# Kernel tuning notes

Measured on AMD Instinct MI355X. Metric: run time of the kernel, lower is better.

Reference implementation:

```python
import jax, jax.numpy as jnp
import numpy as np

B, D, H, W = 1024, 256, 8, 8
NS, ITERS, HID = 8, 5, 256  # HID = max(dim, 128)
EPS = 1e-8


def _ln(x, w, b, axes):
    mu = x.mean(axes, keepdims=True)
    var = x.var(axes, keepdims=True)
    return (x - mu) * jax.lax.rsqrt(var + 1e-5) * w + b


def _grid():
    ranges = [np.linspace(0.0, 1.0, num=r) for r in (H, W)]
    g = np.stack(np.meshgrid(*ranges, indexing='ij'), -1).reshape(H, W, -1)[None].astype(np.float32)
    return jnp.asarray(np.concatenate([g, 1.0 - g], -1))  # [1,H,W,4]


def setup_inputs():
    key = jax.random.key(0)
    ks = jax.random.split(key, 16)
    r = lambda i, shape, s=0.02: jax.random.normal(ks[i], shape, jnp.float32) * s
    d = D
    return {
        'inputs': jax.random.normal(ks[0], (B, D, H, W), jnp.float32),
        'slots_noise': jax.random.normal(ks[1], (B, NS, D), jnp.float32),
        'pos_W': r(2, (4, d)), 'pos_b': jnp.zeros((d,), jnp.float32),
        'enln_w': jnp.ones((H * W, d), jnp.float32), 'enln_b': jnp.zeros((H * W, d), jnp.float32),
        'f1W': r(3, (d, d)), 'f1b': jnp.zeros((d,), jnp.float32),
        'f2W': r(4, (d, d)), 'f2b': jnp.zeros((d,), jnp.float32),
        'ni_w': jnp.ones((d,), jnp.float32), 'ni_b': jnp.zeros((d,), jnp.float32),
        'qW': r(5, (d, d)), 'qb': jnp.zeros((d,), jnp.float32),
        'kW': r(6, (d, d)), 'kb': jnp.zeros((d,), jnp.float32),
        'vW': r(7, (d, d)), 'vb': jnp.zeros((d,), jnp.float32),
        'gih': r(8, (3 * d, d)), 'ghh': r(9, (3 * d, d)),
        'bih': jnp.zeros((3 * d,), jnp.float32), 'bhh': jnp.zeros((3 * d,), jnp.float32),
        'ns_w': jnp.ones((d,), jnp.float32), 'ns_b': jnp.zeros((d,), jnp.float32),
        'pf_w': jnp.ones((d,), jnp.float32), 'pf_b': jnp.zeros((d,), jnp.float32),
        'm1W': r(10, (d, HID)), 'm1b': jnp.zeros((HID,), jnp.float32),
        'm2W': r(11, (HID, d)), 'm2b': jnp.zeros((d,), jnp.float32),
        'slots_mu': r(12, (1, 1, d), 0.1),
        'slots_sigma': r(13, (1, 1, d), 0.1),
    }


def reference(inputs, slots_noise, pos_W, pos_b, enln_w, enln_b, f1W, f1b, f2W, f2b,
              ni_w, ni_b, qW, qb, kW, kb, vW, vb, gih, ghh, bih, bhh,
              ns_w, ns_b, pf_w, pf_b, m1W, m1b, m2W, m2b, slots_mu, slots_sigma):
    b, d = inputs.shape[0], inputs.shape[1]
    scale = d ** -0.5
    # encoder_transformation (position=True)
    x = jnp.transpose(inputs, (0, 2, 3, 1))          # [B,H,W,D]
    x = x + (_grid() @ pos_W + pos_b)                # SoftPositionEmbed
    x = x.reshape(b, H * W, d)                       # flatten spatial -> tokens
    x = _ln(x, enln_w, enln_b, (-2, -1))             # LayerNorm([ntokens, dim])
    x = jax.nn.relu(x @ f1W + f1b)
    x = jax.nn.relu(x @ f2W + f2b)
    x = _ln(x, ni_w, ni_b, (-1,))                    # norm_input
    k = x @ kW + kb                                  # [B,N,D]
    v = x @ vW + vb
    # slot init: torch.normal(mu, exp(0.5*sigma)) with explicit noise
    slots = slots_mu + jnp.exp(0.5 * slots_sigma) * slots_noise  # [B,S,D]
    for _ in range(ITERS):
        slots_prev = slots
        q = _ln(slots, ns_w, ns_b, (-1,)) @ qW + qb
        dots = jnp.einsum('bid,bjd->bij', q, k) * scale  # [B,S,N]
        attn = jax.nn.softmax(dots, axis=1) + EPS        # softmax over SLOT axis
        attn = attn / attn.sum(-1, keepdims=True)        # renormalize over tokens
        updates = jnp.einsum('bjd,bij->bid', v, attn)    # [B,S,D]
        # GRUCell(updates, slots_prev)
        gx = updates @ gih.T + bih
        gh = slots_prev @ ghh.T + bhh
        xr, xz, xn = jnp.split(gx, 3, -1)
        hr, hz, hn = jnp.split(gh, 3, -1)
        r_ = jax.nn.sigmoid(xr + hr)
        z_ = jax.nn.sigmoid(xz + hz)
        n_ = jnp.tanh(xn + r_ * hn)
        slots = (1.0 - z_) * n_ + z_ * slots_prev
        # residual MLP
        h = jax.nn.relu(_ln(slots, pf_w, pf_b, (-1,)) @ m1W + m1b)
        slots = slots + (h @ m2W + m2b)
    return slots
```

## Files before the change

kernel.cpp:

```cpp
#include <hip/hip_runtime.h>
#include <math.h>


typedef __attribute__((ext_vector_type(8))) short short8;
typedef __attribute__((ext_vector_type(4))) float f32x4;
typedef unsigned long long ull;

__device__ __forceinline__ unsigned short f2bf(float f) {
    union { float f; unsigned u; } x; x.f = f;
    unsigned r = x.u + 0x7fffu + ((x.u >> 16) & 1u);
    return (unsigned short)(r >> 16);
}
__device__ __forceinline__ float bf2f(unsigned short h) {
    union { unsigned u; float f; } x; x.u = ((unsigned)h) << 16;
    return x.f;
}
__device__ __forceinline__ float sigmoidf_(float x) { return 1.f / (1.f + expf(-x)); }
__device__ __forceinline__ ull pack4(float a, float b, float c, float d) {
    return (ull)f2bf(a) | ((ull)f2bf(b) << 16) | ((ull)f2bf(c) << 32) | ((ull)f2bf(d) << 48);
}
__device__ __forceinline__ short8 afrag256(const unsigned short* buf, int row, int k) {
    return *(const short8*)(buf + row * 256 + (k ^ ((row & 7) << 3)));
}
__device__ __forceinline__ short8 afrag64(const unsigned short* buf, int row, int k) {
    return *(const short8*)(buf + row * 64 + (k ^ ((row & 7) << 3)));
}

__global__ void convert_weights(
    const float* __restrict__ f1W, const float* __restrict__ f2W,
    const float* __restrict__ kW,  const float* __restrict__ vW,
    const float* __restrict__ qW,  const float* __restrict__ m1W,
    const float* __restrict__ m2W, const float* __restrict__ gih,
    const float* __restrict__ ghh, unsigned short* __restrict__ out)
{
    int id = blockIdx.x * 512 + threadIdx.x;
    if (id < 7 * 65536) {
        int mi = id >> 16, e = id & 65535;
        int k = e >> 8, n = e & 255;
        const float* src = mi == 0 ? f1W : mi == 1 ? f2W : mi == 2 ? kW :
                           mi == 3 ? vW  : mi == 4 ? qW  : mi == 5 ? m1W : m2W;
        out[mi * 65536 + n * 256 + k] = f2bf(src[e]);
    } else if (id < 851968) {
        int e = id - 7 * 65536;
        const float* src = e < 196608 ? gih : ghh;
        int ee = e < 196608 ? e : e - 196608;
        out[458752 + e] = f2bf(src[ee]);
    }
}

__launch_bounds__(512)
__global__ void slot_init(const float* __restrict__ mu, const float* __restrict__ sig,
                          const float* __restrict__ noise,
                          const float* __restrict__ nsw, const float* __restrict__ nsb,
                          float* __restrict__ ping, unsigned short* __restrict__ sraw,
                          unsigned short* __restrict__ lnq)
{
    const int t = threadIdx.x, lane = t & 63, wave = t >> 6;
    const int row = blockIdx.x * 8 + wave;
    const int c = lane * 4;
    float4 n4 = *(const float4*)(noise + (size_t)row * 256 + c);
    float4 m4 = *(const float4*)(mu + c);
    float4 g4 = *(const float4*)(sig + c);
    float v0 = m4.x + expf(0.5f * g4.x) * n4.x;
    float v1 = m4.y + expf(0.5f * g4.y) * n4.y;
    float v2 = m4.z + expf(0.5f * g4.z) * n4.z;
    float v3 = m4.w + expf(0.5f * g4.w) * n4.w;
    float s1 = v0 + v1 + v2 + v3;
    float s2 = v0 * v0 + v1 * v1 + v2 * v2 + v3 * v3;
    #pragma unroll
    for (int m = 32; m >= 1; m >>= 1) { s1 += __shfl_xor(s1, m); s2 += __shfl_xor(s2, m); }
    float mu_ = s1 * (1.f / 256.f);
    float rs_ = rsqrtf(s2 * (1.f / 256.f) - mu_ * mu_ + 1e-5f);
    float4 w4 = *(const float4*)(nsw + c);
    float4 b4 = *(const float4*)(nsb + c);
    *(float4*)(ping + (size_t)row * 256 + c) = make_float4(v0, v1, v2, v3);
    *(ull*)(sraw + (size_t)row * 256 + c) = pack4(v0, v1, v2, v3);
    *(ull*)(lnq + (size_t)row * 256 + c) = pack4(
        (v0 - mu_) * rs_ * w4.x + b4.x, (v1 - mu_) * rs_ * w4.y + b4.y,
        (v2 - mu_) * rs_ * w4.z + b4.z, (v3 - mu_) * rs_ * w4.w + b4.w);
}

__launch_bounds__(512)
__global__ void enc1_kernel(const float* __restrict__ g_in,
                            const float* __restrict__ g_posW, const float* __restrict__ g_posb,
                            const float* __restrict__ g_enw,  const float* __restrict__ g_enb,
                            const unsigned short* __restrict__ f1t,
                            const float* __restrict__ f1b,
                            unsigned short* __restrict__ outB)
{
    __shared__ unsigned short xs[64 * 256];
    __shared__ float red[16];
    const int b = blockIdx.x, t = threadIdx.x, lane = t & 63, wave = t >> 6;

    const float* inb = g_in + (size_t)b * 16384;
    float psum = 0.f, psq = 0.f;
    for (int i = 0; i < 8; ++i) {
        int idx4 = i * 512 + t;
        int d = idx4 >> 4;
        int r0 = (idx4 & 15) << 2;
        float4 v = ((const float4*)inb)[idx4];
        float pw0 = g_posW[d], pw1 = g_posW[256 + d], pw2 = g_posW[512 + d], pw3 = g_posW[768 + d];
        float pb = g_posb[d];
        float vals[4] = {v.x, v.y, v.z, v.w};
        #pragma unroll
        for (int q = 0; q < 4; ++q) {
            int r = r0 + q;
            float fh = (float)(r >> 3) * (1.f / 7.f);
            float fw = (float)(r & 7) * (1.f / 7.f);
            float x = vals[q] + fh * pw0 + fw * pw1 + (1.f - fh) * pw2 + (1.f - fw) * pw3 + pb;
            xs[r * 256 + (d ^ ((r & 7) << 3))] = f2bf(x);
            psum += x; psq += x * x;
        }
    }
    #pragma unroll
    for (int m = 32; m >= 1; m >>= 1) { psum += __shfl_xor(psum, m); psq += __shfl_xor(psq, m); }
    if (lane == 0) { red[wave] = psum; red[8 + wave] = psq; }
    __syncthreads();
    {
        float tsum = 0.f, tsq = 0.f;
        #pragma unroll
        for (int w2 = 0; w2 < 8; ++w2) { tsum += red[w2]; tsq += red[8 + w2]; }
        float mu = tsum * (1.f / 16384.f);
        float rs = rsqrtf(tsq * (1.f / 16384.f) - mu * mu + 1e-5f);
        int row = t >> 3, c0 = (t & 7) * 32;
        for (int j = 0; j < 8; ++j) {
            int c = c0 + j * 4;
            ull* p = (ull*)(xs + row * 256 + (c ^ ((row & 7) << 3)));
            ull pk = *p;
            float4 w4 = *(const float4*)&g_enw[row * 256 + c];
            float4 b4 = *(const float4*)&g_enb[row * 256 + c];
            float v0 = (bf2f((unsigned short)pk)         - mu) * rs * w4.x + b4.x;
            float v1 = (bf2f((unsigned short)(pk >> 16)) - mu) * rs * w4.y + b4.y;
            float v2 = (bf2f((unsigned short)(pk >> 32)) - mu) * rs * w4.z + b4.z;
            float v3 = (bf2f((unsigned short)(pk >> 48)) - mu) * rs * w4.w + b4.w;
            *p = pack4(v0, v1, v2, v3);
        }
    }
    __syncthreads();

    const int lr = lane & 15, lk = (lane >> 4) * 8, mr = (lane >> 4) * 4;
    const int wc = wave * 32;
    short8 w0[8], w1[8];
    {
        const unsigned short* wp0 = f1t + (size_t)(wc + lr) * 256 + lk;
        const unsigned short* wp1 = f1t + (size_t)(wc + 16 + lr) * 256 + lk;
        #pragma unroll
        for (int kk = 0; kk < 8; ++kk) {
            w0[kk] = *(const short8*)(wp0 + kk * 32);
            w1[kk] = *(const short8*)(wp1 + kk * 32);
        }
    }
    const float b0 = f1b[wc + lr], b1 = f1b[wc + 16 + lr];
    for (int mt = 0; mt < 4; ++mt) {
        short8 a[8];
        #pragma unroll
        for (int kk = 0; kk < 8; ++kk) a[kk] = afrag256(xs, mt * 16 + lr, kk * 32 + lk);
        f32x4 acc0 = (f32x4){0.f,0.f,0.f,0.f}, acc1 = (f32x4){0.f,0.f,0.f,0.f};
        #pragma unroll
        for (int kk = 0; kk < 8; ++kk) {
            acc0 = __builtin_amdgcn_mfma_f32_16x16x32_bf16(a[kk], w0[kk], acc0, 0, 0, 0);
            acc1 = __builtin_amdgcn_mfma_f32_16x16x32_bf16(a[kk], w1[kk], acc1, 0, 0, 0);
        }
        #pragma unroll
        for (int r = 0; r < 4; ++r) {
            size_t row = (size_t)b * 64 + mt * 16 + mr + r;
            outB[row * 256 + wc + lr]      = f2bf(fmaxf(acc0[r] + b0, 0.f));
            outB[row * 256 + wc + 16 + lr] = f2bf(fmaxf(acc1[r] + b1, 0.f));
        }
    }
}

__launch_bounds__(512)
__global__ void enc2_kernel(const unsigned short* __restrict__ inB,
                            const unsigned short* __restrict__ f2t, const float* __restrict__ f2b,
                            const float* __restrict__ niw, const float* __restrict__ nib,
                            const unsigned short* __restrict__ kt,  const float* __restrict__ kb,
                            const unsigned short* __restrict__ vwt, const float* __restrict__ vb,
                            unsigned short* __restrict__ ks, unsigned short* __restrict__ vt)
{
    __shared__ unsigned short XL[64 * 256];
    const int b = blockIdx.x, t = threadIdx.x, lane = t & 63, wave = t >> 6;
    const int lr = lane & 15, lk = (lane >> 4) * 8, mr = (lane >> 4) * 4;
    const int wc = wave * 32;

    for (int i = 0; i < 8; ++i) {
        int id = t + 512 * i;
        int row = id >> 6, c4 = (id & 63) * 4;
        *(ull*)(XL + row * 256 + (c4 ^ ((row & 7) << 3))) =
            *(const ull*)(inB + (size_t)b * 16384 + row * 256 + c4);
    }
    __syncthreads();

    f32x4 acc[4][2];
    {
        short8 w0[8], w1[8];
        const unsigned short* wp0 = f2t + (size_t)(wc + lr) * 256 + lk;
        const unsigned short* wp1 = f2t + (size_t)(wc + 16 + lr) * 256 + lk;
        #pragma unroll
        for (int kk = 0; kk < 8; ++kk) {
            w0[kk] = *(const short8*)(wp0 + kk * 32);
            w1[kk] = *(const short8*)(wp1 + kk * 32);
        }
        #pragma unroll
        for (int mt = 0; mt < 4; ++mt) {
            acc[mt][0] = (f32x4){0.f,0.f,0.f,0.f};
            acc[mt][1] = (f32x4){0.f,0.f,0.f,0.f};
            short8 a[8];
            #pragma unroll
            for (int kk = 0; kk < 8; ++kk) a[kk] = afrag256(XL, mt * 16 + lr, kk * 32 + lk);
            #pragma unroll
            for (int kk = 0; kk < 8; ++kk) {
                acc[mt][0] = __builtin_amdgcn_mfma_f32_16x16x32_bf16(a[kk], w0[kk], acc[mt][0], 0, 0, 0);
                acc[mt][1] = __builtin_amdgcn_mfma_f32_16x16x32_bf16(a[kk], w1[kk], acc[mt][1], 0, 0, 0);
            }
        }
    }
    __syncthreads();
    {
        const float b0 = f2b[wc + lr], b1 = f2b[wc + 16 + lr];
        #pragma unroll
        for (int mt = 0; mt < 4; ++mt)
            #pragma unroll
            for (int r = 0; r < 4; ++r) {
                int lrow = mt * 16 + mr + r;
                XL[lrow * 256 + ((wc + lr)      ^ ((lrow & 7) << 3))] = f2bf(fmaxf(acc[mt][0][r] + b0, 0.f));
                XL[lrow * 256 + ((wc + 16 + lr) ^ ((lrow & 7) << 3))] = f2bf(fmaxf(acc[mt][1][r] + b1, 0.f));
            }
    }
    __syncthreads();

    {
        const float4 w4 = *(const float4*)(niw + lane * 4);
        const float4 b4 = *(const float4*)(nib + lane * 4);
        for (int rr = 0; rr < 8; ++rr) {
            int row = wave * 8 + rr;
            ull* p = (ull*)(XL + row * 256 + ((lane * 4) ^ ((row & 7) << 3)));
            ull pk = *p;
            float v0 = bf2f((unsigned short)pk),         v1 = bf2f((unsigned short)(pk >> 16));
            float v2 = bf2f((unsigned short)(pk >> 32)), v3 = bf2f((unsigned short)(pk >> 48));
            float s1 = v0 + v1 + v2 + v3;
            float s2 = v0 * v0 + v1 * v1 + v2 * v2 + v3 * v3;
            #pragma unroll
            for (int m = 32; m >= 1; m >>= 1) { s1 += __shfl_xor(s1, m); s2 += __shfl_xor(s2, m); }
            float mu_ = s1 * (1.f / 256.f);
            float rs_ = rsqrtf(s2 * (1.f / 256.f) - mu_ * mu_ + 1e-5f);
            *p = pack4((v0 - mu_) * rs_ * w4.x + b4.x, (v1 - mu_) * rs_ * w4.y + b4.y,
                       (v2 - mu_) * rs_ * w4.z + b4.z, (v3 - mu_) * rs_ * w4.w + b4.w);
        }
    }
    __syncthreads();

    {
        short8 w0[8], w1[8];
        const unsigned short* wp0 = kt + (size_t)(wc + lr) * 256 + lk;
        const unsigned short* wp1 = kt + (size_t)(wc + 16 + lr) * 256 + lk;
        #pragma unroll
        for (int kk = 0; kk < 8; ++kk) {
            w0[kk] = *(const short8*)(wp0 + kk * 32);
            w1[kk] = *(const short8*)(wp1 + kk * 32);
        }
        const float b0 = kb[wc + lr], b1 = kb[wc + 16 + lr];
        for (int mt = 0; mt < 4; ++mt) {
            short8 a[8];
            #pragma unroll
            for (int kk = 0; kk < 8; ++kk) a[kk] = afrag256(XL, mt * 16 + lr, kk * 32 + lk);
            f32x4 a0 = (f32x4){0.f,0.f,0.f,0.f}, a1 = (f32x4){0.f,0.f,0.f,0.f};
            #pragma unroll
            for (int kk = 0; kk < 8; ++kk) {
                a0 = __builtin_amdgcn_mfma_f32_16x16x32_bf16(a[kk], w0[kk], a0, 0, 0, 0);
                a1 = __builtin_amdgcn_mfma_f32_16x16x32_bf16(a[kk], w1[kk], a1, 0, 0, 0);
            }
            #pragma unroll
            for (int r = 0; r < 4; ++r) {
                size_t row = (size_t)b * 64 + mt * 16 + mr + r;
                ks[row * 256 + wc + lr]      = f2bf(a0[r] + b0);
                ks[row * 256 + wc + 16 + lr] = f2bf(a1[r] + b1);
            }
        }
    }
    {
        short8 w0[8], w1[8];
        const unsigned short* wp0 = vwt + (size_t)(wc + lr) * 256 + lk;
        const unsigned short* wp1 = vwt + (size_t)(wc + 16 + lr) * 256 + lk;
        #pragma unroll
        for (int kk = 0; kk < 8; ++kk) {
            w0[kk] = *(const short8*)(wp0 + kk * 32);
            w1[kk] = *(const short8*)(wp1 + kk * 32);
        }
        const float b0 = vb[wc + lr], b1 = vb[wc + 16 + lr];
        for (int mt = 0; mt < 4; ++mt) {
            short8 a[8];
            #pragma unroll
            for (int kk = 0; kk < 8; ++kk) a[kk] = afrag256(XL, mt * 16 + lr, kk * 32 + lk);
            f32x4 a0 = (f32x4){0.f,0.f,0.f,0.f}, a1 = (f32x4){0.f,0.f,0.f,0.f};
            #pragma unroll
            for (int kk = 0; kk < 8; ++kk) {
                a0 = __builtin_amdgcn_mfma_f32_16x16x32_bf16(a[kk], w0[kk], a0, 0, 0, 0);
                a1 = __builtin_amdgcn_mfma_f32_16x16x32_bf16(a[kk], w1[kk], a1, 0, 0, 0);
            }
            int t0 = mt * 16 + mr;
            *(ull*)(vt + (size_t)b * 16384 + (size_t)(wc + lr) * 64 + t0) =
                pack4(a0[0] + b0, a0[1] + b0, a0[2] + b0, a0[3] + b0);
            *(ull*)(vt + (size_t)b * 16384 + (size_t)(wc + 16 + lr) * 64 + t0) =
                pack4(a1[0] + b1, a1[1] + b1, a1[2] + b1, a1[3] + b1);
        }
    }
}

__launch_bounds__(512)
__global__ void iter_kernel(
    const unsigned short* __restrict__ Kb, const unsigned short* __restrict__ Vtb,
    const unsigned short* __restrict__ qt,
    const unsigned short* __restrict__ gihb, const unsigned short* __restrict__ ghhb,
    const unsigned short* __restrict__ m1t,  const unsigned short* __restrict__ m2t,
    const float* __restrict__ qb,  const float* __restrict__ bih, const float* __restrict__ bhh,
    const float* __restrict__ pfw, const float* __restrict__ pfb,
    const float* __restrict__ m1b, const float* __restrict__ m2b,
    const float* __restrict__ nsw, const float* __restrict__ nsb,
    float* __restrict__ ping, unsigned short* __restrict__ sraw,
    unsigned short* __restrict__ lnq,
    float* __restrict__ outf, int last)
{
    __shared__ unsigned short SA[32 * 256];
    __shared__ unsigned short SS[32 * 256];
    __shared__ unsigned short QP[4][16 * 256];
    __shared__ unsigned short AT[4][16 * 64];
    __shared__ unsigned short US[32 * 256];
    __shared__ float AF[4][8][72];
    __shared__ float HL[32][256];

    const int t = threadIdx.x, lane = t & 63, wave = t >> 6;
    const int m0 = blockIdx.x * 32;
    const int b0 = blockIdx.x * 4;
    const int lr = lane & 15, lk = (lane >> 4) * 8, mr = (lane >> 4) * 4;
    const int wc = wave * 32;

    for (int i = 0; i < 4; ++i) {
        int id = t + 512 * i;
        int row = id >> 6, c4 = (id & 63) * 4;
        size_t g = ((size_t)m0 + row) * 256 + c4;
        int sw = c4 ^ ((row & 7) << 3);
        *(ull*)(SA + row * 256 + sw) = *(const ull*)(lnq + g);
        *(ull*)(SS + row * 256 + sw) = *(const ull*)(sraw + g);
    }
    for (int i = t; i < 2048; i += 512) {
        int bb = i >> 9, rem = i & 511;
        int row = 8 + (rem >> 6), c4 = (rem & 63) * 4;
        *(ull*)(&QP[bb][row * 256 + c4]) = 0;
    }
    for (int i = t; i < 1024; i += 512) ((ull*)AT)[i] = 0;
    __syncthreads();

    {
        short8 w0[8], w1[8];
        const unsigned short* wp0 = qt + (size_t)(wc + lr) * 256 + lk;
        const unsigned short* wp1 = qt + (size_t)(wc + 16 + lr) * 256 + lk;
        #pragma unroll
        for (int kk = 0; kk < 8; ++kk) {
            w0[kk] = *(const short8*)(wp0 + kk * 32);
            w1[kk] = *(const short8*)(wp1 + kk * 32);
        }
        const float bq0 = qb[wc + lr], bq1 = qb[wc + 16 + lr];
        #pragma unroll
        for (int mt = 0; mt < 2; ++mt) {
            short8 a[8];
            #pragma unroll
            for (int kk = 0; kk < 8; ++kk) a[kk] = afrag256(SA, mt * 16 + lr, kk * 32 + lk);
            f32x4 a0 = (f32x4){0.f,0.f,0.f,0.f}, a1 = (f32x4){0.f,0.f,0.f,0.f};
            #pragma unroll
            for (int kk = 0; kk < 8; ++kk) {
                a0 = __builtin_amdgcn_mfma_f32_16x16x32_bf16(a[kk], w0[kk], a0, 0, 0, 0);
                a1 = __builtin_amdgcn_mfma_f32_16x16x32_bf16(a[kk], w1[kk], a1, 0, 0, 0);
            }
            #pragma unroll
            for (int r = 0; r < 4; ++r) {
                int row = mt * 16 + mr + r;
                int bb = row >> 3, sr = row & 7;
                QP[bb][sr * 256 + ((wc + lr)      ^ (sr << 3))] = f2bf(a0[r] + bq0);
                QP[bb][sr * 256 + ((wc + 16 + lr) ^ (sr << 3))] = f2bf(a1[r] + bq1);
            }
        }
    }
    __syncthreads();

    {
        const int bb = wave >> 1, th = wave & 1;
        const int b = b0 + bb;
        short8 af[8];
        #pragma unroll
        for (int kk = 0; kk < 8; ++kk) af[kk] = afrag256(QP[bb], lr, kk * 32 + lk);
        #pragma unroll
        for (int tf = 0; tf < 2; ++tf) {
            int n0 = th * 32 + tf * 16;
            f32x4 acc = (f32x4){0.f,0.f,0.f,0.f};
            const unsigned short* kp = Kb + ((size_t)b * 64 + n0 + lr) * 256 + lk;
            #pragma unroll
            for (int kk = 0; kk < 8; ++kk)
                acc = __builtin_amdgcn_mfma_f32_16x16x32_bf16(af[kk], *(const short8*)(kp + kk * 32), acc, 0, 0, 0);
            #pragma unroll
            for (int r = 0; r < 4; ++r)
                if (mr + r < 8) AF[bb][mr + r][n0 + lr] = acc[r] * 0.0625f;
        }
    }
    __syncthreads();

    if (t < 256) {
        int b2 = t >> 6, tok = t & 63;
        float mx = AF[b2][0][tok];
        #pragma unroll
        for (int s = 1; s < 8; ++s) mx = fmaxf(mx, AF[b2][s][tok]);
        float e[8], den = 0.f;
        #pragma unroll
        for (int s = 0; s < 8; ++s) { e[s] = expf(AF[b2][s][tok] - mx); den += e[s]; }
        float inv = 1.f / den;
        #pragma unroll
        for (int s = 0; s < 8; ++s) AF[b2][s][tok] = e[s] * inv + 1e-8f;
    }
    __syncthreads();

    #pragma unroll
    for (int j = 0; j < 4; ++j) {
        int row = wave * 4 + j;
        int bb = row >> 3, sr = row & 7;
        float v = AF[bb][sr][lane];
        float ssum = v;
        #pragma unroll
        for (int m = 32; m >= 1; m >>= 1) ssum += __shfl_xor(ssum, m);
        AT[bb][sr * 64 + (lane ^ (sr << 3))] = f2bf(v / ssum);
    }
    __syncthreads();

    {
        const int bb = wave >> 1, ch = wave & 1;
        const int b = b0 + bb;
        short8 a0 = afrag64(AT[bb], lr, lk);
        short8 a1 = afrag64(AT[bb], lr, 32 + lk);
        #pragma unroll
        for (int cf = 0; cf < 8; ++cf) {
            int col = ch * 128 + cf * 16 + lr;
            const unsigned short* vp = Vtb + (size_t)b * 16384 + (size_t)col * 64;
            f32x4 acc = (f32x4){0.f,0.f,0.f,0.f};
            acc = __builtin_amdgcn_mfma_f32_16x16x32_bf16(a0, *(const short8*)(vp + lk), acc, 0, 0, 0);
            acc = __builtin_amdgcn_mfma_f32_16x16x32_bf16(a1, *(const short8*)(vp + 32 + lk), acc, 0, 0, 0);
            #pragma unroll
            for (int r = 0; r < 4; ++r)
                if (mr + r < 8) {
                    int row = bb * 8 + mr + r;
                    US[row * 256 + (col ^ ((row & 7) << 3))] = f2bf(acc[r]);
                }
        }
    }
    __syncthreads();

    {
        f32x4 aR[2][2], aZ[2][2], aN[2][2], aH[2][2];
        #pragma unroll
        for (int cf = 0; cf < 2; ++cf)
            #pragma unroll
            for (int m = 0; m < 2; ++m) {
                aR[cf][m] = (f32x4){0.f,0.f,0.f,0.f}; aZ[cf][m] = (f32x4){0.f,0.f,0.f,0.f};
                aN[cf][m] = (f32x4){0.f,0.f,0.f,0.f}; aH[cf][m] = (f32x4){0.f,0.f,0.f,0.f};
            }
        #pragma unroll
        for (int g = 0; g < 3; ++g) {
            #pragma unroll
            for (int cf = 0; cf < 2; ++cf) {
                int col = wc + cf * 16 + lr;
                const unsigned short* px = gihb + (size_t)(g * 256 + col) * 256 + lk;
                const unsigned short* ph = ghhb + (size_t)(g * 256 + col) * 256 + lk;
                short8 wx[8], wh[8];
                #pragma unroll
                for (int kk = 0; kk < 8; ++kk) {
                    wx[kk] = *(const short8*)(px + kk * 32);
                    wh[kk] = *(const short8*)(ph + kk * 32);
                }
                #pragma unroll
                for (int m = 0; m < 2; ++m) {
                    #pragma unroll
                    for (int kk = 0; kk < 8; ++kk) {
                        short8 u = afrag256(US, m * 16 + lr, kk * 32 + lk);
                        short8 s = afrag256(SS, m * 16 + lr, kk * 32 + lk);
                        if (g == 0) {
                            aR[cf][m] = __builtin_amdgcn_mfma_f32_16x16x32_bf16(u, wx[kk], aR[cf][m], 0, 0, 0);
                            aR[cf][m] = __builtin_amdgcn_mfma_f32_16x16x32_bf16(s, wh[kk], aR[cf][m], 0, 0, 0);
                        } else if (g == 1) {
                            aZ[cf][m] = __builtin_amdgcn_mfma_f32_16x16x32_bf16(u, wx[kk], aZ[cf][m], 0, 0, 0);
                            aZ[cf][m] = __builtin_amdgcn_mfma_f32_16x16x32_bf16(s, wh[kk], aZ[cf][m], 0, 0, 0);
                        } else {
                            aN[cf][m] = __builtin_amdgcn_mfma_f32_16x16x32_bf16(u, wx[kk], aN[cf][m], 0, 0, 0);
                            aH[cf][m] = __builtin_amdgcn_mfma_f32_16x16x32_bf16(s, wh[kk], aH[cf][m], 0, 0, 0);
                        }
                    }
                }
            }
        }
        #pragma unroll
        for (int cf = 0; cf < 2; ++cf) {
            int col = wc + cf * 16 + lr;
            float bR  = bih[col] + bhh[col];
            float bZ  = bih[col + 256] + bhh[col + 256];
            float bXN = bih[col + 512], bHN = bhh[col + 512];
            #pragma unroll
            for (int m = 0; m < 2; ++m)
                #pragma unroll
                for (int r = 0; r < 4; ++r) {
                    int row = m * 16 + mr + r;
                    float prev = ping[((size_t)m0 + row) * 256 + col];
                    float rr = sigmoidf_(aR[cf][m][r] + bR);
                    float zz = sigmoidf_(aZ[cf][m][r] + bZ);
                    float nn = tanhf(aN[cf][m][r] + bXN + rr * (aH[cf][m][r] + bHN));
                    HL[row][col] = (1.f - zz) * nn + zz * prev;
                }
        }
    }
    __syncthreads();
    {
        const float4 w4 = *(const float4*)(pfw + lane * 4);
        const float4 b4 = *(const float4*)(pfb + lane * 4);
        #pragma unroll
        for (int rr = 0; rr < 4; ++rr) {
            int row = wave * 4 + rr;
            float4 v = *(const float4*)&HL[row][lane * 4];
            float s1 = v.x + v.y + v.z + v.w;
            float s2 = v.x * v.x + v.y * v.y + v.z * v.z + v.w * v.w;
            #pragma unroll
            for (int m = 32; m >= 1; m >>= 1) { s1 += __shfl_xor(s1, m); s2 += __shfl_xor(s2, m); }
            float mu_ = s1 * (1.f / 256.f);
            float rs_ = rsqrtf(s2 * (1.f / 256.f) - mu_ * mu_ + 1e-5f);
            *(ull*)(SA + row * 256 + ((lane * 4) ^ ((row & 7) << 3))) = pack4(
                (v.x - mu_) * rs_ * w4.x + b4.x, (v.y - mu_) * rs_ * w4.y + b4.y,
                (v.z - mu_) * rs_ * w4.z + b4.z, (v.w - mu_) * rs_ * w4.w + b4.w);
        }
    }
    __syncthreads();

    {
        short8 w0[8], w1[8];
        const unsigned short* wp0 = m1t + (size_t)(wc + lr) * 256 + lk;
        const unsigned short* wp1 = m1t + (size_t)(wc + 16 + lr) * 256 + lk;
        #pragma unroll
        for (int kk = 0; kk < 8; ++kk) {
            w0[kk] = *(const short8*)(wp0 + kk * 32);
            w1[kk] = *(const short8*)(wp1 + kk * 32);
        }
        const float b0 = m1b[wc + lr], b1 = m1b[wc + 16 + lr];
        #pragma unroll
        for (int mt = 0; mt < 2; ++mt) {
            short8 a[8];
            #pragma unroll
            for (int kk = 0; kk < 8; ++kk) a[kk] = afrag256(SA, mt * 16 + lr, kk * 32 + lk);
            f32x4 a0 = (f32x4){0.f,0.f,0.f,0.f}, a1 = (f32x4){0.f,0.f,0.f,0.f};
            #pragma unroll
            for (int kk = 0; kk < 8; ++kk) {
                a0 = __builtin_amdgcn_mfma_f32_16x16x32_bf16(a[kk], w0[kk], a0, 0, 0, 0);
                a1 = __builtin_amdgcn_mfma_f32_16x16x32_bf16(a[kk], w1[kk], a1, 0, 0, 0);
            }
            #pragma unroll
            for (int r = 0; r < 4; ++r) {
                int row = mt * 16 + mr + r;
                US[row * 256 + ((wc + lr)      ^ ((row & 7) << 3))] = f2bf(fmaxf(a0[r] + b0, 0.f));
                US[row * 256 + ((wc + 16 + lr) ^ ((row & 7) << 3))] = f2bf(fmaxf(a1[r] + b1, 0.f));
            }
        }
    }
    __syncthreads();

    {
        short8 w0[8], w1[8];
        const unsigned short* wp0 = m2t + (size_t)(wc + lr) * 256 + lk;
        const unsigned short* wp1 = m2t + (size_t)(wc + 16 + lr) * 256 + lk;
        #pragma unroll
        for (int kk = 0; kk < 8; ++kk) {
            w0[kk] = *(const short8*)(wp0 + kk * 32);
            w1[kk] = *(const short8*)(wp1 + kk * 32);
        }
        const float b0 = m2b[wc + lr], b1 = m2b[wc + 16 + lr];
        #pragma unroll
        for (int mt = 0; mt < 2; ++mt) {
            short8 a[8];
            #pragma unroll
            for (int kk = 0; kk < 8; ++kk) a[kk] = afrag256(US, mt * 16 + lr, kk * 32 + lk);
            f32x4 a0 = (f32x4){0.f,0.f,0.f,0.f}, a1 = (f32x4){0.f,0.f,0.f,0.f};
            #pragma unroll
            for (int kk = 0; kk < 8; ++kk) {
                a0 = __builtin_amdgcn_mfma_f32_16x16x32_bf16(a[kk], w0[kk], a0, 0, 0, 0);
                a1 = __builtin_amdgcn_mfma_f32_16x16x32_bf16(a[kk], w1[kk], a1, 0, 0, 0);
            }
            #pragma unroll
            for (int r = 0; r < 4; ++r) {
                int row = mt * 16 + mr + r;
                HL[row][wc + lr]      = a0[r] + b0 + HL[row][wc + lr];
                HL[row][wc + 16 + lr] = a1[r] + b1 + HL[row][wc + 16 + lr];
            }
        }
    }
    __syncthreads();
    {
        const float4 w4 = *(const float4*)(nsw + lane * 4);
        const float4 b4 = *(const float4*)(nsb + lane * 4);
        #pragma unroll
        for (int rr = 0; rr < 4; ++rr) {
            int row = wave * 4 + rr;
            size_t off = ((size_t)m0 + row) * 256 + lane * 4;
            float4 v = *(const float4*)&HL[row][lane * 4];
            if (last) {
                *(float4*)(outf + off) = v;
            } else {
                float s1 = v.x + v.y + v.z + v.w;
                float s2 = v.x * v.x + v.y * v.y + v.z * v.z + v.w * v.w;
                #pragma unroll
                for (int m = 32; m >= 1; m >>= 1) { s1 += __shfl_xor(s1, m); s2 += __shfl_xor(s2, m); }
                float mu_ = s1 * (1.f / 256.f);
                float rs_ = rsqrtf(s2 * (1.f / 256.f) - mu_ * mu_ + 1e-5f);
                *(float4*)(ping + off) = v;
                *(ull*)(sraw + off) = pack4(v.x, v.y, v.z, v.w);
                *(ull*)(lnq + off) = pack4(
                    (v.x - mu_) * rs_ * w4.x + b4.x, (v.y - mu_) * rs_ * w4.y + b4.y,
                    (v.z - mu_) * rs_ * w4.z + b4.z, (v.w - mu_) * rs_ * w4.w + b4.w);
            }
        }
    }
}

extern "C" void kernel_launch(void* const* d_in, const int* in_sizes, int n_in,
                              void* d_out, int out_size, void* d_ws, size_t ws_size,
                              hipStream_t stream) {
    (void)in_sizes; (void)n_in; (void)ws_size; (void)out_size;
    unsigned short* wsb  = (unsigned short*)d_ws;
    unsigned short* bufB = wsb + (1u << 20);
    unsigned short* ksb  = bufB + 16777216;
    unsigned short* vtb  = ksb + 16777216;
    float* ping = (float*)(vtb + 16777216);
    unsigned short* srawb = (unsigned short*)(ping + 2097152);
    unsigned short* lnqb  = srawb + 2097152;

    const unsigned short* f1t  = wsb;
    const unsigned short* f2t  = wsb + 65536;
    const unsigned short* kt   = wsb + 131072;
    const unsigned short* vwt  = wsb + 196608;
    const unsigned short* qt   = wsb + 262144;
    const unsigned short* m1t  = wsb + 327680;
    const unsigned short* m2t  = wsb + 393216;
    const unsigned short* gihb = wsb + 458752;
    const unsigned short* ghhb = wsb + 655360;

    convert_weights<<<dim3(1664), dim3(512), 0, stream>>>(
        (const float*)d_in[6],  (const float*)d_in[8],  (const float*)d_in[14],
        (const float*)d_in[16], (const float*)d_in[12], (const float*)d_in[26],
        (const float*)d_in[28], (const float*)d_in[18], (const float*)d_in[19], wsb);

    enc1_kernel<<<dim3(1024), dim3(512), 0, stream>>>(
        (const float*)d_in[0], (const float*)d_in[2], (const float*)d_in[3],
        (const float*)d_in[4], (const float*)d_in[5],
        f1t, (const float*)d_in[7], bufB);

    enc2_kernel<<<dim3(1024), dim3(512), 0, stream>>>(
        bufB, f2t, (const float*)d_in[9],
        (const float*)d_in[10], (const float*)d_in[11],
        kt, (const float*)d_in[15], vwt, (const float*)d_in[17],
        ksb, vtb);

    slot_init<<<dim3(1024), dim3(512), 0, stream>>>(
        (const float*)d_in[30], (const float*)d_in[31], (const float*)d_in[1],
        (const float*)d_in[22], (const float*)d_in[23], ping, srawb, lnqb);

    for (int it = 0; it < 5; ++it) {
        iter_kernel<<<dim3(256), dim3(512), 0, stream>>>(
            ksb, vtb, qt, gihb, ghhb, m1t, m2t,
            (const float*)d_in[13], (const float*)d_in[20], (const float*)d_in[21],
            (const float*)d_in[24], (const float*)d_in[25],
            (const float*)d_in[27], (const float*)d_in[29],
            (const float*)d_in[22], (const float*)d_in[23],
            ping, srawb, lnqb,
            (float*)d_out, it == 4 ? 1 : 0);
    }
}
```

Before: 440.7 us.

## Split slot-attention iteration into separate attention and GRU/MLP kernels

The fused per-iteration kernel is split in two. An attention kernel runs 512 blocks of 256 threads, each covering 2 batches: it computes the q projection, the dots with K, the slot-axis softmax, the token renormalisation and the update with V, then writes bf16 updates to a workspace buffer. A GRU/MLP kernel keeps the original 256-block grid and reads those updates from global memory. The aim is more blocks and lower LDS use for the attention part, which reads a lot of K/V, so more of the chip is busy. The cost is an extra kernel launch and a global round trip for the updates on each iteration.

```diff
diff --git a/kernel.cpp b/kernel.cpp
--- a/kernel.cpp
+++ b/kernel.cpp
@@ -307,13 +307,128 @@
     }
 }
 
+__launch_bounds__(256)
+__global__ void attn_kernel(
+    const unsigned short* __restrict__ Kb, const unsigned short* __restrict__ Vtb,
+    const unsigned short* __restrict__ qt, const float* __restrict__ qb,
+    const unsigned short* __restrict__ lnq,
+    unsigned short* __restrict__ upd)
+{
+    __shared__ unsigned short QP[2][16 * 256];
+    __shared__ unsigned short AT[2][16 * 64];
+    __shared__ float AF[2][8][72];
+
+    const int t = threadIdx.x, lane = t & 63, wave = t >> 6;
+    const int m0 = blockIdx.x * 16;
+    const int b0 = blockIdx.x * 2;
+    const int lr = lane & 15, lk = (lane >> 4) * 8, mr = (lane >> 4) * 4;
+
+    for (int i = t; i < 1024; i += 256) {
+        int bb = i >> 9, rem = i & 511;
+        int row = 8 + (rem >> 6), c4 = (rem & 63) * 4;
+        *(ull*)(&QP[bb][row * 256 + c4]) = 0;
+    }
+    ((ull*)AT)[t] = 0;
+    ((ull*)AT)[t + 256] = 0;
+    __syncthreads();
+
+    {
+        short8 a[8];
+        const unsigned short* ap = lnq + (size_t)(m0 + lr) * 256 + lk;
+        #pragma unroll
+        for (int kk = 0; kk < 8; ++kk) a[kk] = *(const short8*)(ap + kk * 32);
+        #pragma unroll
+        for (int f = 0; f < 4; ++f) {
+            int col = wave * 64 + f * 16 + lr;
+            const unsigned short* wp = qt + (size_t)col * 256 + lk;
+            f32x4 acc = (f32x4){0.f,0.f,0.f,0.f};
+            #pragma unroll
+            for (int kk = 0; kk < 8; ++kk)
+                acc = __builtin_amdgcn_mfma_f32_16x16x32_bf16(a[kk], *(const short8*)(wp + kk * 32), acc, 0, 0, 0);
+            float bq = qb[col];
+            #pragma unroll
+            for (int r = 0; r < 4; ++r) {
+                int row = mr + r;
+                int bb = row >> 3, sr = row & 7;
+                QP[bb][sr * 256 + (col ^ (sr << 3))] = f2bf(acc[r] + bq);
+            }
+        }
+    }
+    __syncthreads();
+
+    {
+        const int bb = wave >> 1, th = wave & 1;
+        const int b = b0 + bb;
+        short8 af[8];
+        #pragma unroll
+        for (int kk = 0; kk < 8; ++kk) af[kk] = afrag256(QP[bb], lr, kk * 32 + lk);
+        #pragma unroll
+        for (int tf = 0; tf < 2; ++tf) {
+            int n0 = th * 32 + tf * 16;
+            f32x4 acc = (f32x4){0.f,0.f,0.f,0.f};
+            const unsigned short* kp = Kb + ((size_t)b * 64 + n0 + lr) * 256 + lk;
+            #pragma unroll
+            for (int kk = 0; kk < 8; ++kk)
+                acc = __builtin_amdgcn_mfma_f32_16x16x32_bf16(af[kk], *(const short8*)(kp + kk * 32), acc, 0, 0, 0);
+            #pragma unroll
+            for (int r = 0; r < 4; ++r)
+                if (mr + r < 8) AF[bb][mr + r][n0 + lr] = acc[r] * 0.0625f;
+        }
+    }
+    __syncthreads();
+
+    if (t < 128) {
+        int b2 = t >> 6, tok = t & 63;
+        float mx = AF[b2][0][tok];
+        #pragma unroll
+        for (int s = 1; s < 8; ++s) mx = fmaxf(mx, AF[b2][s][tok]);
+        float e[8], den = 0.f;
+        #pragma unroll
+        for (int s = 0; s < 8; ++s) { e[s] = expf(AF[b2][s][tok] - mx); den += e[s]; }
+        float inv = 1.f / den;
+        #pragma unroll
+        for (int s = 0; s < 8; ++s) AF[b2][s][tok] = e[s] * inv + 1e-8f;
+    }
+    __syncthreads();
+
+    #pragma unroll
+    for (int j = 0; j < 4; ++j) {
+        int row = wave * 4 + j;
+        int bb = row >> 3, sr = row & 7;
+        float v = AF[bb][sr][lane];
+        float ssum = v;
+        #pragma unroll
+        for (int m = 32; m >= 1; m >>= 1) ssum += __shfl_xor(ssum, m);
+        AT[bb][sr * 64 + (lane ^ (sr << 3))] = f2bf(v / ssum);
+    }
+    __syncthreads();
+
+    {
+        const int bb = wave >> 1, ch = wave & 1;
+        const int b = b0 + bb;
+        short8 a0 = afrag64(AT[bb], lr, lk);
+        short8 a1 = afrag64(AT[bb], lr, 32 + lk);
+        #pragma unroll
+        for (int cf = 0; cf < 8; ++cf) {
+            int col = ch * 128 + cf * 16 + lr;
+            const unsigned short* vp = Vtb + (size_t)b * 16384 + (size_t)col * 64;
+            f32x4 acc = (f32x4){0.f,0.f,0.f,0.f};
+            acc = __builtin_amdgcn_mfma_f32_16x16x32_bf16(a0, *(const short8*)(vp + lk), acc, 0, 0, 0);
+            acc = __builtin_amdgcn_mfma_f32_16x16x32_bf16(a1, *(const short8*)(vp + 32 + lk), acc, 0, 0, 0);
+            #pragma unroll
+            for (int r = 0; r < 4; ++r)
+                if (mr + r < 8)
+                    upd[((size_t)b * 8 + mr + r) * 256 + col] = f2bf(acc[r]);
+        }
+    }
+}
+
 __launch_bounds__(512)
-__global__ void iter_kernel(
-    const unsigned short* __restrict__ Kb, const unsigned short* __restrict__ Vtb,
-    const unsigned short* __restrict__ qt,
+__global__ void gru_kernel(
+    const unsigned short* __restrict__ upd,
     const unsigned short* __restrict__ gihb, const unsigned short* __restrict__ ghhb,
     const unsigned short* __restrict__ m1t,  const unsigned short* __restrict__ m2t,
-    const float* __restrict__ qb,  const float* __restrict__ bih, const float* __restrict__ bhh,
+    const float* __restrict__ bih, const float* __restrict__ bhh,
     const float* __restrict__ pfw, const float* __restrict__ pfb,
     const float* __restrict__ m1b, const float* __restrict__ m2b,
     const float* __restrict__ nsw, const float* __restrict__ nsb,
@@ -321,17 +436,13 @@
     unsigned short* __restrict__ lnq,
     float* __restrict__ outf, int last)
 {
+    __shared__ unsigned short SS[32 * 256];
+    __shared__ unsigned short US[32 * 256];
     __shared__ unsigned short SA[32 * 256];
-    __shared__ unsigned short SS[32 * 256];
-    __shared__ unsigned short QP[4][16 * 256];
-    __shared__ unsigned short AT[4][16 * 64];
-    __shared__ unsigned short US[32 * 256];
-    __shared__ float AF[4][8][72];
     __shared__ float HL[32][256];
 
     const int t = threadIdx.x, lane = t & 63, wave = t >> 6;
     const int m0 = blockIdx.x * 32;
-    const int b0 = blockIdx.x * 4;
     const int lr = lane & 15, lk = (lane >> 4) * 8, mr = (lane >> 4) * 4;
     const int wc = wave * 32;
 
@@ -340,115 +451,8 @@
         int row = id >> 6, c4 = (id & 63) * 4;
         size_t g = ((size_t)m0 + row) * 256 + c4;
         int sw = c4 ^ ((row & 7) << 3);
-        *(ull*)(SA + row * 256 + sw) = *(const ull*)(lnq + g);
+        *(ull*)(US + row * 256 + sw) = *(const ull*)(upd + g);
         *(ull*)(SS + row * 256 + sw) = *(const ull*)(sraw + g);
-    }
-    for (int i = t; i < 2048; i += 512) {
-        int bb = i >> 9, rem = i & 511;
-        int row = 8 + (rem >> 6), c4 = (rem & 63) * 4;
-        *(ull*)(&QP[bb][row * 256 + c4]) = 0;
-    }
-    for (int i = t; i < 1024; i += 512) ((ull*)AT)[i] = 0;
-    __syncthreads();
-
-    {
-        short8 w0[8], w1[8];
-        const unsigned short* wp0 = qt + (size_t)(wc + lr) * 256 + lk;
-        const unsigned short* wp1 = qt + (size_t)(wc + 16 + lr) * 256 + lk;
-        #pragma unroll
-        for (int kk = 0; kk < 8; ++kk) {
-            w0[kk] = *(const short8*)(wp0 + kk * 32);
-            w1[kk] = *(const short8*)(wp1 + kk * 32);
-        }
-        const float bq0 = qb[wc + lr], bq1 = qb[wc + 16 + lr];
-        #pragma unroll
-        for (int mt = 0; mt < 2; ++mt) {
-            short8 a[8];
-            #pragma unroll
-            for (int kk = 0; kk < 8; ++kk) a[kk] = afrag256(SA, mt * 16 + lr, kk * 32 + lk);
-            f32x4 a0 = (f32x4){0.f,0.f,0.f,0.f}, a1 = (f32x4){0.f,0.f,0.f,0.f};
-            #pragma unroll
-            for (int kk = 0; kk < 8; ++kk) {
-                a0 = __builtin_amdgcn_mfma_f32_16x16x32_bf16(a[kk], w0[kk], a0, 0, 0, 0);
-                a1 = __builtin_amdgcn_mfma_f32_16x16x32_bf16(a[kk], w1[kk], a1, 0, 0, 0);
-            }
-            #pragma unroll
-            for (int r = 0; r < 4; ++r) {
-                int row = mt * 16 + mr + r;
-                int bb = row >> 3, sr = row & 7;
-                QP[bb][sr * 256 + ((wc + lr)      ^ (sr << 3))] = f2bf(a0[r] + bq0);
-                QP[bb][sr * 256 + ((wc + 16 + lr) ^ (sr << 3))] = f2bf(a1[r] + bq1);
-            }
-        }
-    }
-    __syncthreads();
-
-    {
-        const int bb = wave >> 1, th = wave & 1;
-        const int b = b0 + bb;
-        short8 af[8];
-        #pragma unroll
-        for (int kk = 0; kk < 8; ++kk) af[kk] = afrag256(QP[bb], lr, kk * 32 + lk);
-        #pragma unroll
-        for (int tf = 0; tf < 2; ++tf) {
-            int n0 = th * 32 + tf * 16;
-            f32x4 acc = (f32x4){0.f,0.f,0.f,0.f};
-            const unsigned short* kp = Kb + ((size_t)b * 64 + n0 + lr) * 256 + lk;
-            #pragma unroll
-            for (int kk = 0; kk < 8; ++kk)
-                acc = __builtin_amdgcn_mfma_f32_16x16x32_bf16(af[kk], *(const short8*)(kp + kk * 32), acc, 0, 0, 0);
-            #pragma unroll
-            for (int r = 0; r < 4; ++r)
-                if (mr + r < 8) AF[bb][mr + r][n0 + lr] = acc[r] * 0.0625f;
-        }
-    }
-    __syncthreads();
-
-    if (t < 256) {
-        int b2 = t >> 6, tok = t & 63;
-        float mx = AF[b2][0][tok];
-        #pragma unroll
-        for (int s = 1; s < 8; ++s) mx = fmaxf(mx, AF[b2][s][tok]);
-        float e[8], den = 0.f;
-        #pragma unroll
-        for (int s = 0; s < 8; ++s) { e[s] = expf(AF[b2][s][tok] - mx); den += e[s]; }
-        float inv = 1.f / den;
-        #pragma unroll
-        for (int s = 0; s < 8; ++s) AF[b2][s][tok] = e[s] * inv + 1e-8f;
-    }
-    __syncthreads();
-
-    #pragma unroll
-    for (int j = 0; j < 4; ++j) {
-        int row = wave * 4 + j;
-        int bb = row >> 3, sr = row & 7;
-        float v = AF[bb][sr][lane];
-        float ssum = v;
-        #pragma unroll
-        for (int m = 32; m >= 1; m >>= 1) ssum += __shfl_xor(ssum, m);
-        AT[bb][sr * 64 + (lane ^ (sr << 3))] = f2bf(v / ssum);
-    }
-    __syncthreads();
-
-    {
-        const int bb = wave >> 1, ch = wave & 1;
-        const int b = b0 + bb;
-        short8 a0 = afrag64(AT[bb], lr, lk);
-        short8 a1 = afrag64(AT[bb], lr, 32 + lk);
-        #pragma unroll
-        for (int cf = 0; cf < 8; ++cf) {
-            int col = ch * 128 + cf * 16 + lr;
-            const unsigned short* vp = Vtb + (size_t)b * 16384 + (size_t)col * 64;
-            f32x4 acc = (f32x4){0.f,0.f,0.f,0.f};
-            acc = __builtin_amdgcn_mfma_f32_16x16x32_bf16(a0, *(const short8*)(vp + lk), acc, 0, 0, 0);
-            acc = __builtin_amdgcn_mfma_f32_16x16x32_bf16(a1, *(const short8*)(vp + 32 + lk), acc, 0, 0, 0);
-            #pragma unroll
-            for (int r = 0; r < 4; ++r)
-                if (mr + r < 8) {
-                    int row = bb * 8 + mr + r;
-                    US[row * 256 + (col ^ ((row & 7) << 3))] = f2bf(acc[r]);
-                }
-        }
     }
     __syncthreads();
 
@@ -595,29 +599,33 @@
         }
     }
     __syncthreads();
-    {
+
+    if (last) {
+        #pragma unroll
+        for (int rr = 0; rr < 4; ++rr) {
+            int row = wave * 4 + rr;
+            *(float4*)(outf + ((size_t)m0 + row) * 256 + lane * 4) =
+                *(const float4*)&HL[row][lane * 4];
+        }
+    } else {
         const float4 w4 = *(const float4*)(nsw + lane * 4);
         const float4 b4 = *(const float4*)(nsb + lane * 4);
         #pragma unroll
         for (int rr = 0; rr < 4; ++rr) {
             int row = wave * 4 + rr;
+            float4 v = *(const float4*)&HL[row][lane * 4];
+            float s1 = v.x + v.y + v.z + v.w;
+            float s2 = v.x * v.x + v.y * v.y + v.z * v.z + v.w * v.w;
+            #pragma unroll
+            for (int m = 32; m >= 1; m >>= 1) { s1 += __shfl_xor(s1, m); s2 += __shfl_xor(s2, m); }
+            float mu_ = s1 * (1.f / 256.f);
+            float rs_ = rsqrtf(s2 * (1.f / 256.f) - mu_ * mu_ + 1e-5f);
             size_t off = ((size_t)m0 + row) * 256 + lane * 4;
-            float4 v = *(const float4*)&HL[row][lane * 4];
-            if (last) {
-                *(float4*)(outf + off) = v;
-            } else {
-                float s1 = v.x + v.y + v.z + v.w;
-                float s2 = v.x * v.x + v.y * v.y + v.z * v.z + v.w * v.w;
-                #pragma unroll
-                for (int m = 32; m >= 1; m >>= 1) { s1 += __shfl_xor(s1, m); s2 += __shfl_xor(s2, m); }
-                float mu_ = s1 * (1.f / 256.f);
-                float rs_ = rsqrtf(s2 * (1.f / 256.f) - mu_ * mu_ + 1e-5f);
-                *(float4*)(ping + off) = v;
-                *(ull*)(sraw + off) = pack4(v.x, v.y, v.z, v.w);
-                *(ull*)(lnq + off) = pack4(
-                    (v.x - mu_) * rs_ * w4.x + b4.x, (v.y - mu_) * rs_ * w4.y + b4.y,
-                    (v.z - mu_) * rs_ * w4.z + b4.z, (v.w - mu_) * rs_ * w4.w + b4.w);
-            }
+            *(float4*)(ping + off) = v;
+            *(ull*)(sraw + off) = pack4(v.x, v.y, v.z, v.w);
+            *(ull*)(lnq + off) = pack4(
+                (v.x - mu_) * rs_ * w4.x + b4.x, (v.y - mu_) * rs_ * w4.y + b4.y,
+                (v.z - mu_) * rs_ * w4.z + b4.z, (v.w - mu_) * rs_ * w4.w + b4.w);
         }
     }
 }
@@ -633,6 +641,7 @@
     float* ping = (float*)(vtb + 16777216);
     unsigned short* srawb = (unsigned short*)(ping + 2097152);
     unsigned short* lnqb  = srawb + 2097152;
+    unsigned short* updb  = bufB + 8388608;
 
     const unsigned short* f1t  = wsb;
     const unsigned short* f2t  = wsb + 65536;
@@ -665,9 +674,11 @@
         (const float*)d_in[22], (const float*)d_in[23], ping, srawb, lnqb);
 
     for (int it = 0; it < 5; ++it) {
-        iter_kernel<<<dim3(256), dim3(512), 0, stream>>>(
-            ksb, vtb, qt, gihb, ghhb, m1t, m2t,
-            (const float*)d_in[13], (const float*)d_in[20], (const float*)d_in[21],
+        attn_kernel<<<dim3(512), dim3(256), 0, stream>>>(
+            ksb, vtb, qt, (const float*)d_in[13], lnqb, updb);
+        gru_kernel<<<dim3(256), dim3(512), 0, stream>>>(
+            updb, gihb, ghhb, m1t, m2t,
+            (const float*)d_in[20], (const float*)d_in[21],
             (const float*)d_in[24], (const float*)d_in[25],
             (const float*)d_in[27], (const float*)d_in[29],
             (const float*)d_in[22], (const float*)d_in[23],
```

Measured after the change: 469.6 us. +6.6%, slower.
